# Kernel optimization log

Hardware: AMD Instinct MI355X
Metric: run time of the kernel (lower is better)

Reference implementation:

```python
import jax, jax.numpy as jnp
import numpy as np
from jax import lax

DIM = 2048
K = 3


def rms_norm(x):
    eps = jnp.asarray(jnp.finfo(x.dtype).eps, x.dtype)
    var = jnp.mean(jnp.square(x), axis=-1, keepdims=True)
    return x * lax.rsqrt(var + eps)


def causal_dwconv1d(y, w, b, dilation):
    # y: [B, S, D]; w: [D, 1, K]; depthwise causal conv along S
    yc = jnp.transpose(y, (0, 2, 1))  # [B, D, S]
    pad = (K - 1) * dilation
    out = lax.conv_general_dilated(
        yc, w.astype(yc.dtype),
        window_strides=(1,),
        padding=[(pad, 0)],
        rhs_dilation=(dilation,),
        dimension_numbers=('NCH', 'OIH', 'NCH'),
        feature_group_count=DIM,
    )
    out = out + b.astype(yc.dtype)[None, :, None]
    return jnp.transpose(out, (0, 2, 1))  # [B, S, D]


def setup_inputs() -> dict:
    key = jax.random.key(0)
    ks = jax.random.split(key, 4)
    B, S, D = 4, 4096, DIM
    x = jax.random.normal(ks[0], (B, S, D), dtype=jnp.float32)
    W_expand = jax.random.normal(ks[1], (3 * D, D), dtype=jnp.float32) * (1.0 / np.sqrt(D))
    conv_w = jax.random.normal(ks[2], (D, 1, K), dtype=jnp.float32) * (1.0 / K)
    conv_b = jnp.zeros((D,), dtype=jnp.float32)
    W_proj = jax.random.normal(ks[3], (D, D), dtype=jnp.float32) * (1.0 / np.sqrt(D))
    conv_scale = jnp.ones((D,), dtype=jnp.float32)
    return {"x": x, "W_expand": W_expand, "conv_w": conv_w, "conv_b": conv_b,
            "W_proj": W_proj, "conv_scale": conv_scale, "dilation": 1}


def reference(x, W_expand, conv_w, conv_b, W_proj, conv_scale, dilation):
    h = jnp.einsum('bsd,ed->bse', rms_norm(x), W_expand.astype(x.dtype))
    B_gate, C_gate, z = jnp.split(h, 3, axis=-1)
    y = B_gate * z  # squared_gate=False
    y = causal_dwconv1d(y, conv_w, conv_b, dilation)
    o = C_gate * y
    o = jnp.einsum('bsd,ed->bse', o, W_proj.astype(x.dtype))
    return x + conv_scale.astype(x.dtype)[None, None, :] * o
```

## Files before the change

kernel.cpp:

```cpp
#include <hip/hip_runtime.h>
#include <hip/hip_bf16.h>
#include <stdint.h>

typedef __bf16 bf16;
typedef __bf16 bf16x8 __attribute__((ext_vector_type(8)));
typedef __bf16 bf16x4 __attribute__((ext_vector_type(4)));
typedef float  floatx4 __attribute__((ext_vector_type(4)));

#define DIMD 2048
#define BATB 4
#define SEQS 4096
#define MTOT (BATB*SEQS)

#define BAR()   __builtin_amdgcn_s_barrier()
#define LGKM0() asm volatile("s_waitcnt lgkmcnt(0)" ::: "memory")
#define LGKM8() asm volatile("s_waitcnt lgkmcnt(8)" ::: "memory")
#define VMC6()  asm volatile("s_waitcnt vmcnt(6)" ::: "memory")
#define VMC0()  asm volatile("s_waitcnt vmcnt(0)" ::: "memory")
#define SCHED0() __builtin_amdgcn_sched_barrier(0)

__device__ __forceinline__ void gload_lds16(const bf16* g, bf16* l) {
    __builtin_amdgcn_global_load_lds(
        (const __attribute__((address_space(1))) void*)g,
        (__attribute__((address_space(3))) void*)l,
        16, 0, 0);
}

__global__ __launch_bounds__(256) void f2bf_k(const float* __restrict__ src,
                                              bf16* __restrict__ dst, int n) {
    int i = (blockIdx.x * 256 + threadIdx.x) * 4;
    if (i >= n) return;
    float4 v = *(const float4*)&src[i];
    bf16x4 o;
    o[0] = (bf16)v.x; o[1] = (bf16)v.y; o[2] = (bf16)v.z; o[3] = (bf16)v.w;
    *(bf16x4*)&dst[i] = o;
}

__global__ __launch_bounds__(256) void rmsnorm_k(const float* __restrict__ x,
                                                 bf16* __restrict__ xn) {
    const int row = blockIdx.x;
    const int tid = threadIdx.x;
    const float* xr = x + (size_t)row * DIMD;
    float4 a = *(const float4*)&xr[tid * 8];
    float4 b = *(const float4*)&xr[tid * 8 + 4];
    float s = a.x*a.x + a.y*a.y + a.z*a.z + a.w*a.w
            + b.x*b.x + b.y*b.y + b.z*b.z + b.w*b.w;
    #pragma unroll
    for (int off = 32; off > 0; off >>= 1) s += __shfl_down(s, off);
    __shared__ float red[4];
    if ((tid & 63) == 0) red[tid >> 6] = s;
    __syncthreads();
    float tot = red[0] + red[1] + red[2] + red[3];
    float sc = rsqrtf(tot * (1.0f / DIMD) + 1.1920929e-07f);
    bf16x8 o;
    o[0] = (bf16)(a.x * sc); o[1] = (bf16)(a.y * sc);
    o[2] = (bf16)(a.z * sc); o[3] = (bf16)(a.w * sc);
    o[4] = (bf16)(b.x * sc); o[5] = (bf16)(b.y * sc);
    o[6] = (bf16)(b.z * sc); o[7] = (bf16)(b.w * sc);
    *(bf16x8*)&xn[(size_t)row * DIMD + tid * 8] = o;
}

__global__ __launch_bounds__(256) void gateconv_k(const bf16* __restrict__ h,
                                                  const float* __restrict__ cw,
                                                  const float* __restrict__ cb,
                                                  bf16* __restrict__ o,
                                                  const int* __restrict__ dil_p) {
    int gid = blockIdx.x * 256 + threadIdx.x;
    int m = gid >> 9;
    int d = (gid & 511) << 2;
    int s = m & (SEQS - 1);
    int dil = dil_p[0];
    const bf16* hr = h + (size_t)m * (3 * DIMD);

    bf16x4 Cv = *(const bf16x4*)&hr[DIMD + d];
    bf16x4 B0 = *(const bf16x4*)&hr[d];
    bf16x4 Z0 = *(const bf16x4*)&hr[2 * DIMD + d];
    float y0[4], y1[4], y2[4];
    #pragma unroll
    for (int j = 0; j < 4; ++j) y0[j] = (float)B0[j] * (float)Z0[j];
    if (s >= dil) {
        const bf16* h1 = hr - (size_t)dil * 3 * DIMD;
        bf16x4 B1 = *(const bf16x4*)&h1[d];
        bf16x4 Z1 = *(const bf16x4*)&h1[2 * DIMD + d];
        #pragma unroll
        for (int j = 0; j < 4; ++j) y1[j] = (float)B1[j] * (float)Z1[j];
    } else {
        #pragma unroll
        for (int j = 0; j < 4; ++j) y1[j] = 0.0f;
    }
    if (s >= 2 * dil) {
        const bf16* h2 = hr - (size_t)(2 * dil) * 3 * DIMD;
        bf16x4 B2 = *(const bf16x4*)&h2[d];
        bf16x4 Z2 = *(const bf16x4*)&h2[2 * DIMD + d];
        #pragma unroll
        for (int j = 0; j < 4; ++j) y2[j] = (float)B2[j] * (float)Z2[j];
    } else {
        #pragma unroll
        for (int j = 0; j < 4; ++j) y2[j] = 0.0f;
    }
    bf16x4 ov;
    #pragma unroll
    for (int j = 0; j < 4; ++j) {
        float w0 = cw[(d + j) * 3 + 0];
        float w1 = cw[(d + j) * 3 + 1];
        float w2 = cw[(d + j) * 3 + 2];
        float conv = w0 * y2[j] + w1 * y1[j] + w2 * y0[j] + cb[d + j];
        ov[j] = (bf16)((float)Cv[j] * conv);
    }
    *(bf16x4*)&o[(size_t)m * DIMD + d] = ov;
}

template<int RESID>
__global__ __launch_bounds__(512, 2) void gemm_bt(const bf16* __restrict__ A,
                                                  const bf16* __restrict__ B,
                                                  bf16* __restrict__ Hout,
                                                  float* __restrict__ Fout,
                                                  const float* __restrict__ resid,
                                                  const float* __restrict__ scale,
                                                  int M, int N, int K) {
    __shared__ __align__(16) bf16 smem[2][32768];
    const int tid = threadIdx.x;
    const int wave = tid >> 6;
    const int lane = tid & 63;
    const int quad = lane >> 4;
    const int col16 = lane & 15;

    const int nx   = (int)gridDim.x;
    const int nwg  = nx * (int)gridDim.y;
    const int orig = (int)blockIdx.y * nx + (int)blockIdx.x;
    const int lin  = (orig & 7) * (nwg >> 3) + (orig >> 3);
    const int n0 = (lin % nx) * 256;
    const int m0 = (lin / nx) * 256;

    const int wm = (wave >> 2) * 128;
    const int wn = (wave & 3) * 64;

    const int srow = tid >> 3;
    const int cs   = (tid & 7) ^ (srow & 7);
    const bf16* aSrc = A + (size_t)(m0 + srow) * K + cs * 8;
    const bf16* bSrc = B + (size_t)(n0 + srow) * K + cs * 8;
    const int stbase = wave * 512;
    const size_t K64  = (size_t)K * 64;
    const size_t K128 = (size_t)K * 128;

    const int rsw = col16 & 7;
    const int ard = (wm + col16) * 64;
    const int brd = (wn + col16) * 64;
    const int sl0 = ((0 + quad) ^ rsw) * 8;
    const int sl1 = ((4 + quad) ^ rsw) * 8;

    floatx4 acc[4][2][4];
    #pragma unroll
    for (int q = 0; q < 4; ++q)
        #pragma unroll
        for (int f = 0; f < 2; ++f)
            #pragma unroll
            for (int n = 0; n < 4; ++n) acc[q][f][n] = (floatx4)0.0f;

    auto stage = [&](const bf16* src, bf16* dstBase, int t, int h) {
        const bf16* s = src + (size_t)h * K128 + (size_t)t * 64;
        bf16* d = dstBase + h * 8192 + stbase;
        gload_lds16(s, d);
        gload_lds16(s + K64, d + 4096);
    };
    auto lda2 = [&](bf16x8 (&q)[2][2], const bf16* Asb, int f0) {
        #pragma unroll
        for (int f = 0; f < 2; ++f) {
            const bf16* p = Asb + ard + (f0 + f) * (16 * 64);
            q[f][0] = *(const bf16x8*)(p + sl0);
            q[f][1] = *(const bf16x8*)(p + sl1);
        }
    };
    auto ldb4 = [&](bf16x8 (&q)[4][2], const bf16* Bsb) {
        #pragma unroll
        for (int n = 0; n < 4; ++n) {
            const bf16* p = Bsb + brd + n * (16 * 64);
            q[n][0] = *(const bf16x8*)(p + sl0);
            q[n][1] = *(const bf16x8*)(p + sl1);
        }
    };
    auto mm = [&](floatx4 (&ac)[2][4], bf16x8 (&a)[2][2], bf16x8 (&b)[4][2]) {
        __builtin_amdgcn_s_setprio(1);
        #pragma unroll
        for (int f = 0; f < 2; ++f)
            #pragma unroll
            for (int n = 0; n < 4; ++n) {
                ac[f][n] = __builtin_amdgcn_mfma_f32_16x16x32_bf16(a[f][0], b[n][0], ac[f][n], 0, 0, 0);
                ac[f][n] = __builtin_amdgcn_mfma_f32_16x16x32_bf16(a[f][1], b[n][1], ac[f][n], 0, 0, 0);
            }
        __builtin_amdgcn_s_setprio(0);
    };

    const int NT = K >> 6;

    stage(aSrc, smem[0],         0, 0);
    stage(aSrc, smem[0],         0, 1);
    stage(bSrc, smem[0] + 16384, 0, 0);
    stage(bSrc, smem[0] + 16384, 0, 1);
    stage(bSrc, smem[1] + 16384, 1, 0);
    stage(bSrc, smem[1] + 16384, 1, 1);
    stage(aSrc, smem[1],         1, 0);
    VMC6();
    BAR();

    for (int t = 0; t < NT - 2; ++t) {
        const int b = t & 1;
        const bf16* Asb = smem[b];
        const bf16* Bsb = smem[b] + 16384;
        bf16* Asw = smem[b];
        bf16* Bsw = smem[b] + 16384;
        bf16* Aso = smem[b ^ 1];
        bf16x8 bfr[4][2], A0[2][2], A1[2][2], A2[2][2], A3[2][2];
        ldb4(bfr, Bsb);
        lda2(A0, Asb, 0);
        stage(aSrc, Aso, t + 1, 1);
        LGKM8();
        BAR(); LGKM0(); SCHED0();
        mm(acc[0], A0, bfr);
        BAR();
        lda2(A1, Asb, 2);
        lda2(A2, Asb, 4);
        stage(bSrc, Bsw, t + 2, 0);
        BAR(); LGKM0(); SCHED0();
        mm(acc[1], A1, bfr);
        BAR();
        lda2(A3, Asb, 6);
        stage(bSrc, Bsw, t + 2, 1);
        BAR(); LGKM0(); SCHED0();
        mm(acc[2], A2, bfr);
        BAR();
        stage(aSrc, Asw, t + 2, 0);
        VMC6();
        BAR();
        mm(acc[3], A3, bfr);
        BAR();
    }
    {
        const int t = NT - 2;
        const int b = t & 1;
        const bf16* Asb = smem[b];
        const bf16* Bsb = smem[b] + 16384;
        bf16* Aso = smem[b ^ 1];
        bf16x8 bfr[4][2], A0[2][2], A1[2][2], A2[2][2], A3[2][2];
        ldb4(bfr, Bsb);
        lda2(A0, Asb, 0);
        stage(aSrc, Aso, t + 1, 1);
        LGKM8();
        BAR(); LGKM0(); SCHED0();
        mm(acc[0], A0, bfr);
        BAR();
        lda2(A1, Asb, 2);
        lda2(A2, Asb, 4);
        BAR(); LGKM0(); SCHED0();
        mm(acc[1], A1, bfr);
        BAR();
        lda2(A3, Asb, 6);
        BAR(); LGKM0(); SCHED0();
        mm(acc[2], A2, bfr);
        BAR();
        VMC0();
        BAR();
        mm(acc[3], A3, bfr);
        BAR();
    }
    {
        const int b = (NT - 1) & 1;
        const bf16* Asb = smem[b];
        const bf16* Bsb = smem[b] + 16384;
        bf16x8 bfr[4][2], A0[2][2], A1[2][2], A2[2][2], A3[2][2];
        ldb4(bfr, Bsb);
        lda2(A0, Asb, 0);
        BAR(); LGKM0(); SCHED0();
        mm(acc[0], A0, bfr);
        BAR();
        lda2(A1, Asb, 2);
        lda2(A2, Asb, 4);
        BAR(); LGKM0(); SCHED0();
        mm(acc[1], A1, bfr);
        BAR();
        lda2(A3, Asb, 6);
        BAR(); LGKM0(); SCHED0();
        mm(acc[2], A2, bfr);
        mm(acc[3], A3, bfr);
    }

    #pragma unroll
    for (int q2 = 0; q2 < 4; ++q2)
        #pragma unroll
        for (int f = 0; f < 2; ++f)
            #pragma unroll
            for (int n = 0; n < 4; ++n) {
                const int c  = n0 + wn + n * 16 + col16;
                const int rb = m0 + wm + (q2 * 2 + f) * 16 + quad * 4;
                #pragma unroll
                for (int r = 0; r < 4; ++r) {
                    size_t off = (size_t)(rb + r) * N + c;
                    float v = acc[q2][f][n][r];
                    if (RESID) {
                        Fout[off] = resid[off] + scale[c] * v;
                    } else {
                        Hout[off] = (bf16)v;
                    }
                }
            }
}

extern "C" void kernel_launch(void* const* d_in, const int* in_sizes, int n_in,
                              void* d_out, int out_size, void* d_ws, size_t ws_size,
                              hipStream_t stream) {
    const float* x  = (const float*)d_in[0];
    const float* We = (const float*)d_in[1];
    const float* cw = (const float*)d_in[2];
    const float* cb = (const float*)d_in[3];
    const float* Wp = (const float*)d_in[4];
    const float* cs = (const float*)d_in[5];
    const int*   dil = (const int*)d_in[6];

    char* ws = (char*)d_ws;
    bf16* xn  = (bf16*)ws;
    bf16* Web = (bf16*)(ws + 67108864);
    bf16* Wpb = (bf16*)(ws + 67108864 + 25165824);
    bf16* h   = (bf16*)(ws + 100663296);

    f2bf_k<<<(3 * DIMD * DIMD / 4 + 255) / 256, 256, 0, stream>>>(We, Web, 3 * DIMD * DIMD);
    f2bf_k<<<(DIMD * DIMD / 4 + 255) / 256, 256, 0, stream>>>(Wp, Wpb, DIMD * DIMD);
    rmsnorm_k<<<MTOT, 256, 0, stream>>>(x, xn);
    gemm_bt<0><<<dim3(3 * DIMD / 256, MTOT / 256), 512, 0, stream>>>(
        xn, Web, h, nullptr, nullptr, nullptr, MTOT, 3 * DIMD, DIMD);
    gateconv_k<<<(MTOT * (DIMD / 4)) / 256, 256, 0, stream>>>(h, cw, cb, xn , dil);
    gemm_bt<1><<<dim3(DIMD / 256, MTOT / 256), 512, 0, stream>>>(
        xn , Wpb, nullptr, (float*)d_out, x, cs, MTOT, DIMD, DIMD);
}
```

Measured before the change: 829.9 us.

## Software-pipeline LDS fragment loads one phase ahead of MFMA in GEMM loop

Restructures the GEMM main loop so each phase's A fragment (and the next tile's B and A0 fragments) is read from LDS one phase ahead of the MFMAs that use it. The blanket lgkmcnt(0) waits become partial waits. The aim is to overlap LDS read latency with matrix-core work instead of stalling at each barrier. This needs more live fragment registers, and the waitcnt values must stay correct alongside the interleaved global-to-LDS loads.

```diff
diff --git a/kernel.cpp b/kernel.cpp
--- a/kernel.cpp
+++ b/kernel.cpp
@@ -12,11 +12,10 @@
 #define SEQS 4096
 #define MTOT (BATB*SEQS)
 
-#define BAR()   __builtin_amdgcn_s_barrier()
-#define LGKM0() asm volatile("s_waitcnt lgkmcnt(0)" ::: "memory")
-#define LGKM8() asm volatile("s_waitcnt lgkmcnt(8)" ::: "memory")
-#define VMC6()  asm volatile("s_waitcnt vmcnt(6)" ::: "memory")
-#define VMC0()  asm volatile("s_waitcnt vmcnt(0)" ::: "memory")
+#define BAR()    __builtin_amdgcn_s_barrier()
+#define LGKMC(N) asm volatile("s_waitcnt lgkmcnt(" #N ")" ::: "memory")
+#define VMC6()   asm volatile("s_waitcnt vmcnt(6)" ::: "memory")
+#define VMC0()   asm volatile("s_waitcnt vmcnt(0)" ::: "memory")
 #define SCHED0() __builtin_amdgcn_sched_barrier(0)
 
 __device__ __forceinline__ void gload_lds16(const bf16* g, bf16* l) {
@@ -149,6 +148,8 @@
     const int sl0 = ((0 + quad) ^ rsw) * 8;
     const int sl1 = ((4 + quad) ^ rsw) * 8;
 
+    bf16x8 Bf[4][2];
+    bf16x8 A0[2][2], A1[2][2], A2[2][2], A3[2][2];
     floatx4 acc[4][2][4];
     #pragma unroll
     for (int q = 0; q < 4; ++q)
@@ -163,7 +164,7 @@
         gload_lds16(s, d);
         gload_lds16(s + K64, d + 4096);
     };
-    auto lda2 = [&](bf16x8 (&q)[2][2], const bf16* Asb, int f0) {
+    auto ldA = [&](bf16x8 (&q)[2][2], const bf16* Asb, int f0) {
         #pragma unroll
         for (int f = 0; f < 2; ++f) {
             const bf16* p = Asb + ard + (f0 + f) * (16 * 64);
@@ -171,22 +172,22 @@
             q[f][1] = *(const bf16x8*)(p + sl1);
         }
     };
-    auto ldb4 = [&](bf16x8 (&q)[4][2], const bf16* Bsb) {
+    auto ldB = [&](const bf16* Bsb) {
         #pragma unroll
         for (int n = 0; n < 4; ++n) {
             const bf16* p = Bsb + brd + n * (16 * 64);
-            q[n][0] = *(const bf16x8*)(p + sl0);
-            q[n][1] = *(const bf16x8*)(p + sl1);
+            Bf[n][0] = *(const bf16x8*)(p + sl0);
+            Bf[n][1] = *(const bf16x8*)(p + sl1);
         }
     };
-    auto mm = [&](floatx4 (&ac)[2][4], bf16x8 (&a)[2][2], bf16x8 (&b)[4][2]) {
+    auto mm = [&](floatx4 (&ac)[2][4], bf16x8 (&a)[2][2]) {
         __builtin_amdgcn_s_setprio(1);
         #pragma unroll
         for (int f = 0; f < 2; ++f)
             #pragma unroll
             for (int n = 0; n < 4; ++n) {
-                ac[f][n] = __builtin_amdgcn_mfma_f32_16x16x32_bf16(a[f][0], b[n][0], ac[f][n], 0, 0, 0);
-                ac[f][n] = __builtin_amdgcn_mfma_f32_16x16x32_bf16(a[f][1], b[n][1], ac[f][n], 0, 0, 0);
+                ac[f][n] = __builtin_amdgcn_mfma_f32_16x16x32_bf16(a[f][0], Bf[n][0], ac[f][n], 0, 0, 0);
+                ac[f][n] = __builtin_amdgcn_mfma_f32_16x16x32_bf16(a[f][1], Bf[n][1], ac[f][n], 0, 0, 0);
             }
         __builtin_amdgcn_s_setprio(0);
     };
@@ -202,86 +203,87 @@
     stage(aSrc, smem[1],         1, 0);
     VMC6();
     BAR();
+    ldB(smem[0] + 16384);
+    ldA(A0, smem[0], 0);
+    SCHED0();
 
     for (int t = 0; t < NT - 2; ++t) {
         const int b = t & 1;
-        const bf16* Asb = smem[b];
-        const bf16* Bsb = smem[b] + 16384;
-        bf16* Asw = smem[b];
-        bf16* Bsw = smem[b] + 16384;
-        bf16* Aso = smem[b ^ 1];
-        bf16x8 bfr[4][2], A0[2][2], A1[2][2], A2[2][2], A3[2][2];
-        ldb4(bfr, Bsb);
-        lda2(A0, Asb, 0);
-        stage(aSrc, Aso, t + 1, 1);
-        LGKM8();
-        BAR(); LGKM0(); SCHED0();
-        mm(acc[0], A0, bfr);
-        BAR();
-        lda2(A1, Asb, 2);
-        lda2(A2, Asb, 4);
-        stage(bSrc, Bsw, t + 2, 0);
-        BAR(); LGKM0(); SCHED0();
-        mm(acc[1], A1, bfr);
-        BAR();
-        lda2(A3, Asb, 6);
-        stage(bSrc, Bsw, t + 2, 1);
-        BAR(); LGKM0(); SCHED0();
-        mm(acc[2], A2, bfr);
-        BAR();
-        stage(aSrc, Asw, t + 2, 0);
+        const bf16* Acur = smem[b];
+        bf16* Awr = smem[b];
+        bf16* Bwr = smem[b] + 16384;
+        bf16* Aoth = smem[b ^ 1];
+        const bf16* Anxt = smem[b ^ 1];
+        const bf16* Bnxt = smem[b ^ 1] + 16384;
+        ldA(A1, Acur, 2);
+        stage(aSrc, Aoth, t + 1, 1);
+        SCHED0(); BAR(); LGKMC(4); SCHED0();
+        mm(acc[0], A0);
+        BAR();
+        ldA(A2, Acur, 4);
+        stage(bSrc, Bwr, t + 2, 0);
+        SCHED0(); BAR(); LGKMC(4); SCHED0();
+        mm(acc[1], A1);
+        BAR();
+        ldA(A3, Acur, 6);
+        stage(bSrc, Bwr, t + 2, 1);
+        SCHED0(); BAR(); LGKMC(4); SCHED0();
+        mm(acc[2], A2);
+        BAR();
+        stage(aSrc, Awr, t + 2, 0);
         VMC6();
-        BAR();
-        mm(acc[3], A3, bfr);
-        BAR();
+        BAR(); LGKMC(0); SCHED0();
+        mm(acc[3], A3);
+        SCHED0();
+        ldB(Bnxt);
+        ldA(A0, Anxt, 0);
+        SCHED0(); BAR();
     }
     {
         const int t = NT - 2;
         const int b = t & 1;
-        const bf16* Asb = smem[b];
-        const bf16* Bsb = smem[b] + 16384;
-        bf16* Aso = smem[b ^ 1];
-        bf16x8 bfr[4][2], A0[2][2], A1[2][2], A2[2][2], A3[2][2];
-        ldb4(bfr, Bsb);
-        lda2(A0, Asb, 0);
-        stage(aSrc, Aso, t + 1, 1);
-        LGKM8();
-        BAR(); LGKM0(); SCHED0();
-        mm(acc[0], A0, bfr);
-        BAR();
-        lda2(A1, Asb, 2);
-        lda2(A2, Asb, 4);
-        BAR(); LGKM0(); SCHED0();
-        mm(acc[1], A1, bfr);
-        BAR();
-        lda2(A3, Asb, 6);
-        BAR(); LGKM0(); SCHED0();
-        mm(acc[2], A2, bfr);
+        const bf16* Acur = smem[b];
+        bf16* Aoth = smem[b ^ 1];
+        const bf16* Anxt = smem[b ^ 1];
+        const bf16* Bnxt = smem[b ^ 1] + 16384;
+        ldA(A1, Acur, 2);
+        stage(aSrc, Aoth, t + 1, 1);
+        SCHED0(); BAR(); LGKMC(4); SCHED0();
+        mm(acc[0], A0);
+        BAR();
+        ldA(A2, Acur, 4);
+        SCHED0(); BAR(); LGKMC(4); SCHED0();
+        mm(acc[1], A1);
+        BAR();
+        ldA(A3, Acur, 6);
+        SCHED0(); BAR(); LGKMC(4); SCHED0();
+        mm(acc[2], A2);
         BAR();
         VMC0();
-        BAR();
-        mm(acc[3], A3, bfr);
-        BAR();
+        BAR(); LGKMC(0); SCHED0();
+        mm(acc[3], A3);
+        SCHED0();
+        ldB(Bnxt);
+        ldA(A0, Anxt, 0);
+        SCHED0(); BAR();
     }
     {
         const int b = (NT - 1) & 1;
-        const bf16* Asb = smem[b];
-        const bf16* Bsb = smem[b] + 16384;
-        bf16x8 bfr[4][2], A0[2][2], A1[2][2], A2[2][2], A3[2][2];
-        ldb4(bfr, Bsb);
-        lda2(A0, Asb, 0);
-        BAR(); LGKM0(); SCHED0();
-        mm(acc[0], A0, bfr);
-        BAR();
-        lda2(A1, Asb, 2);
-        lda2(A2, Asb, 4);
-        BAR(); LGKM0(); SCHED0();
-        mm(acc[1], A1, bfr);
-        BAR();
-        lda2(A3, Asb, 6);
-        BAR(); LGKM0(); SCHED0();
-        mm(acc[2], A2, bfr);
-        mm(acc[3], A3, bfr);
+        const bf16* Acur = smem[b];
+        ldA(A1, Acur, 2);
+        SCHED0(); BAR(); LGKMC(4); SCHED0();
+        mm(acc[0], A0);
+        BAR();
+        ldA(A2, Acur, 4);
+        SCHED0(); BAR(); LGKMC(4); SCHED0();
+        mm(acc[1], A1);
+        BAR();
+        ldA(A3, Acur, 6);
+        SCHED0(); BAR(); LGKMC(4); SCHED0();
+        mm(acc[2], A2);
+        BAR();
+        LGKMC(0); SCHED0();
+        mm(acc[3], A3);
     }
 
     #pragma unroll
```

After: 836.9 us. About the same (+0.8%).
